# Performance work log

Hardware: AMD Instinct MI355X
Metric: run time of the kernel (lower is better)

The kernel has to match this reference:

```python
import jax, jax.numpy as jnp
import numpy as np

HIDDEN = 128   # hidden_dim == input_dim (embedding feeds LSTMCell directly)
OUT = 200000   # output_dim: item catalog size
T = 64         # num_timesteps
K = 50         # num_recommendations
HIST = 200     # length of user history x


def setup_inputs() -> dict:
    key = jax.random.key(0)
    ks = jax.random.split(key, 6)
    s = 0.02
    return {
        "x": jax.random.randint(ks[0], (HIST,), 1, OUT + 1),  # 1-indexed items
        "embed_table": jax.random.normal(ks[1], (OUT, HIDDEN), jnp.float32) * s,
        "W_ih": jax.random.normal(ks[2], (4 * HIDDEN, HIDDEN), jnp.float32) * s,
        "W_hh": jax.random.normal(ks[3], (4 * HIDDEN, HIDDEN), jnp.float32) * s,
        "b_ih": jnp.zeros((4 * HIDDEN,), jnp.float32),
        "b_hh": jnp.zeros((4 * HIDDEN,), jnp.float32),
        "W_out": jax.random.normal(ks[4], (OUT, HIDDEN), jnp.float32) * s,
        "b_out": jnp.zeros((OUT,), jnp.float32),
    }


def reference(x, embed_table, W_ih, W_hh, b_ih, b_hh, W_out, b_out):
    # Faithful translation of RecModel.forward with prev_a_hat=None, prev_feedback=None.
    def step(carry, i):
        h, c, mask, a_hat, feedback = carry
        # at i==0 the embedding input is forced to zeros (feedback starts at 0 anyway)
        emb = jnp.where(i > 0, embed_table[a_hat] * feedback.astype(jnp.float32), 0.0)
        # LSTMCell: gates order (input, forget, cell, output) as in torch
        gates = W_ih @ emb + b_ih + W_hh @ h + b_hh
        ig, fg, gg, og = jnp.split(gates, 4)
        c_new = jax.nn.sigmoid(fg) * c + jax.nn.sigmoid(ig) * jnp.tanh(gg)
        h_new = jax.nn.sigmoid(og) * jnp.tanh(c_new)
        probs = jax.nn.softmax(W_out @ h_new + b_out)  # Softmax(dim=0) on [OUT]
        masked = probs * mask
        _, top_items = jax.lax.top_k(masked, K)
        hit = jnp.isin(top_items + 1, x)               # x is 1-indexed
        any_hit = jnp.any(hit)
        first_hit = top_items[jnp.argmax(hit)]         # first intersecting item
        a_new = jnp.where(any_hit, first_hit, top_items[0]).astype(jnp.int32)
        fb_new = jnp.where(any_hit, 1, -1).astype(jnp.int32)
        mask_new = mask.at[a_new].set(0.0)
        return (h_new, c_new, mask_new, a_new, fb_new), (a_new, fb_new, masked)

    init = (
        jnp.zeros((HIDDEN,), jnp.float32),
        jnp.zeros((HIDDEN,), jnp.float32),
        jnp.ones((OUT,), jnp.float32),
        jnp.array(0, jnp.int32),
        jnp.array(0, jnp.int32),
    )
    _, (a_hats, feedbacks, masked_probs) = jax.lax.scan(step, init, jnp.arange(T))
    return a_hats, feedbacks, masked_probs
```

## Files before the change

### kernel.cpp

```cpp
#include <hip/hip_runtime.h>
#include <stdint.h>

#define OUTN   200000
#define HID    128
#define NSTEP  64
#define KTOP   50
#define NBINS  1024
#define CAP    4096
#define NBLK   256
#define NTHR   512
#define NWRD   6250

__device__ __forceinline__ float    gldf(const float* p){ return __hip_atomic_load(p, __ATOMIC_RELAXED, __HIP_MEMORY_SCOPE_AGENT); }
__device__ __forceinline__ void     gstf(float* p, float v){ __hip_atomic_store(p, v, __ATOMIC_RELAXED, __HIP_MEMORY_SCOPE_AGENT); }
__device__ __forceinline__ unsigned gldu(const unsigned* p){ return __hip_atomic_load(p, __ATOMIC_RELAXED, __HIP_MEMORY_SCOPE_AGENT); }
__device__ __forceinline__ void     gstu(unsigned* p, unsigned v){ __hip_atomic_store(p, v, __ATOMIC_RELAXED, __HIP_MEMORY_SCOPE_AGENT); }

__device__ __forceinline__ float dot128f(const float* __restrict__ w, const float* __restrict__ h){
  const float4* w4 = (const float4*)w;
  float acc = 0.f;
  #pragma unroll
  for (int k=0;k<32;k++){
    float4 q = w4[k];
    const float* hp = h + k*4;
    acc += q.x*hp[0] + q.y*hp[1] + q.z*hp[2] + q.w*hp[3];
  }
  return acc;
}

__device__ __forceinline__ int binOf(float l, float rlo, float rsc){
  float b = (l - rlo) * rsc;
  b = fminf(fmaxf(b, 0.f), (float)(NBINS-1));
  return (int)b;
}

__device__ __forceinline__ void blockRed5(float& mx, float& mn, float& a, float& b, float& c,
                                          int tid, float* sm ){
  #pragma unroll
  for (int o=32;o;o>>=1){
    mx=fmaxf(mx,__shfl_xor(mx,o)); mn=fminf(mn,__shfl_xor(mn,o));
    a+=__shfl_xor(a,o); b+=__shfl_xor(b,o); c+=__shfl_xor(c,o);
  }
  __syncthreads();
  if ((tid&63)==0){ int w=tid>>6; sm[w*5+0]=mx; sm[w*5+1]=mn; sm[w*5+2]=a; sm[w*5+3]=b; sm[w*5+4]=c; }
  __syncthreads();
  int nw = blockDim.x>>6;
  if (tid==0){
    for (int k=1;k<nw;k++){
      sm[0]=fmaxf(sm[0],sm[k*5+0]); sm[1]=fminf(sm[1],sm[k*5+1]);
      sm[2]+=sm[k*5+2]; sm[3]+=sm[k*5+3]; sm[4]+=sm[k*5+4];
    }
  }
  __syncthreads();
  mx=sm[0]; mn=sm[1]; a=sm[2]; b=sm[3]; c=sm[4];
}

__device__ __forceinline__ void blockRedPair(float& p, int& i, int tid, float* smp, int* smi){
  __syncthreads();
  #pragma unroll
  for (int o=32;o;o>>=1){
    float p2=__shfl_xor(p,o); int i2=__shfl_xor(i,o);
    if (p2>p || (p2==p && i2<i)){ p=p2; i=i2; }
  }
  if ((tid&63)==0){ smp[tid>>6]=p; smi[tid>>6]=i; }
  __syncthreads();
  if (tid==0){
    for (int k=1;k<8;k++){
      if (smp[k]>smp[0] || (smp[k]==smp[0] && smi[k]<smi[0])){ smp[0]=smp[k]; smi[0]=smi[k]; }
    }
  }
  __syncthreads();
  p=smp[0]; i=smi[0];
}

__device__ __forceinline__ int blockRedSum(int v, int tid, int* smi){
  __syncthreads();
  #pragma unroll
  for (int o=32;o;o>>=1) v += __shfl_xor(v,o);
  if ((tid&63)==0) smi[tid>>6]=v;
  __syncthreads();
  if (tid==0){ int s=0; for(int k=0;k<8;k++) s+=smi[k]; smi[0]=s; }
  __syncthreads();
  return smi[0];
}

__device__ __forceinline__ void histSelect(unsigned* histL, unsigned* csum, int tid, int K, int* outp){
  int base = NBINS - 2*(tid+1);
  csum[tid] = histL[base] + histL[base+1];
  __syncthreads();
  for (int off=1; off<NTHR; off<<=1){
    unsigned add = (tid>=off) ? csum[tid-off] : 0u;
    __syncthreads();
    csum[tid] += add;
    __syncthreads();
  }
  unsigned pre = (tid==0)?0u:csum[tid-1];
  if (csum[tid] >= (unsigned)K && pre < (unsigned)K){
    unsigned run = pre; int bs = base;
    for (int b=base+1; b>=base; --b){
      run += histL[b];
      if (run >= (unsigned)K){ bs=b; break; }
    }
    outp[0]=bs; outp[1]=(int)run;
  }
  __syncthreads();
}

__device__ __forceinline__ void gsync(unsigned* bar, unsigned target){
  asm volatile("s_waitcnt vmcnt(0) lgkmcnt(0)" ::: "memory");
  __syncthreads();
  if (threadIdx.x==0){
    __hip_atomic_fetch_add(bar, 1u, __ATOMIC_RELAXED, __HIP_MEMORY_SCOPE_AGENT);
    unsigned v;
    do {
      __builtin_amdgcn_s_sleep(2);
      v = __hip_atomic_load(bar, __ATOMIC_RELAXED, __HIP_MEMORY_SCOPE_AGENT);
    } while (v < target);
  }
  __syncthreads();
  asm volatile("" ::: "memory");
}

extern "C" __global__ void k_init(const int* __restrict__ x,
                                  const float* __restrict__ b_ih, const float* __restrict__ b_hh,
                                  unsigned* mask_bits, unsigned* inx_bits, unsigned* hist_g,
                                  unsigned* gcount, float* rparams, float* h_ws, float* c_ws,
                                  unsigned* bar)
{
  int tid = threadIdx.x;
  for (int i=tid;i<NWRD;i+=1024){ mask_bits[i]=0xFFFFFFFFu; inx_bits[i]=0u; }
  for (int i=tid;i<NBINS;i+=1024) hist_g[i]=0u;
  if (tid==0){ *gcount=0u; rparams[0]=0.f; rparams[1]=0.f; *bar=0u; }
  if (tid<HID){
    float ig=b_ih[tid]       +b_hh[tid];
    float gg=b_ih[tid+2*HID] +b_hh[tid+2*HID];
    float og=b_ih[tid+3*HID] +b_hh[tid+3*HID];
    float si=1.f/(1.f+expf(-ig)), so=1.f/(1.f+expf(-og));
    float cn=si*tanhf(gg);
    c_ws[tid]=cn; h_ws[tid]=so*tanhf(cn);
  }
  __syncthreads();
  if (tid<200){
    int v = x[tid]-1;
    if (v>=0 && v<OUTN) atomicOr(&inx_bits[v>>5], 1u<<(v&31));
  }
}

struct FusedP {
  const float* emb;  const float* Wih;  const float* Whh;
  const float* bih;  const float* bhh;  const float* Wout; const float* bout;
  float* out;
  float* l_ws; float* partials;
  unsigned* mask_bits; unsigned* inx_bits; unsigned* hist_g;
  unsigned* cand; unsigned* gcount; float* rparams;
  float* h_ws; float* c_ws; unsigned* bar;
};

extern "C" __global__ void __launch_bounds__(NTHR) k_fused(FusedP p)
{
  __shared__ float    h_l[HID];
  __shared__ float    emb_l[HID];
  __shared__ float    gates[4*HID];
  __shared__ unsigned hl[NBINS];
  __shared__ unsigned csum[NTHR];
  __shared__ float    smf[48];
  __shared__ float    smp[8];
  __shared__ int      smi[8];
  __shared__ int      s_sel[2];
  __shared__ int      s_nc, s_cnt;

  const int tid=threadIdx.x, bid=blockIdx.x;
  const int start = bid*781 + (bid<64 ? bid : 64);
  const int cnt   = 781 + (bid<64 ? 1 : 0);
  unsigned barT = 0;

  for (int t=0; t<NSTEP; ++t){
    if (tid<HID) h_l[tid]=gldf(&p.h_ws[tid]);
    for (int i=tid;i<NBINS;i+=NTHR) hl[i]=0u;
    float rlo = gldf(&p.rparams[0]), rsc = gldf(&p.rparams[1]);
    __syncthreads();
    float mx=-3e38f, mn=3e38f, se=0.f, sl=0.f, sl2=0.f;
    float lv0=0.f, lv1=0.f; unsigned mv0=0u, mv1=0u;
    {
      int j = tid;
      if (j < cnt){
        int row = start+j;
        float l = dot128f(p.Wout+(size_t)row*HID, h_l) + p.bout[row];
        gstf(&p.l_ws[row], l);
        lv0 = l;
        se += expf(l)-1.f; sl += l; sl2 += l*l;
        if ((gldu(&p.mask_bits[row>>5])>>(row&31))&1u){
          mv0 = 1u;
          mx=fmaxf(mx,l); mn=fminf(mn,l);
          if (rsc>0.f) atomicAdd(&hl[binOf(l,rlo,rsc)],1u);
        }
      }
      j = tid + NTHR;
      if (j < cnt){
        int row = start+j;
        float l = dot128f(p.Wout+(size_t)row*HID, h_l) + p.bout[row];
        gstf(&p.l_ws[row], l);
        lv1 = l;
        se += expf(l)-1.f; sl += l; sl2 += l*l;
        if ((gldu(&p.mask_bits[row>>5])>>(row&31))&1u){
          mv1 = 1u;
          mx=fmaxf(mx,l); mn=fminf(mn,l);
          if (rsc>0.f) atomicAdd(&hl[binOf(l,rlo,rsc)],1u);
        }
      }
    }
    blockRed5(mx,mn,se,sl,sl2,tid,smf);
    if (tid==0){
      float* q=&p.partials[bid*8];
      gstf(q+0,mx); gstf(q+1,mn); gstf(q+2,se); gstf(q+3,sl); gstf(q+4,sl2);
    }
    if (rsc>0.f){
      for (int i=tid;i<NBINS;i+=NTHR){ unsigned v=hl[i]; if (v) atomicAdd(&p.hist_g[i],v); }
    }
    barT += NBLK; gsync(p.bar, barT);

    if (!(rsc>0.f)){
      float bmx=-3e38f,bmn=3e38f,bse=0.f,bsl=0.f,bsl2=0.f;
      if (tid<NBLK){
        const float* q=&p.partials[tid*8];
        bmx=gldf(q+0); bmn=gldf(q+1); bse=gldf(q+2); bsl=gldf(q+3); bsl2=gldf(q+4);
      }
      blockRed5(bmx,bmn,bse,bsl,bsl2,tid,smf);
      float mean=bsl/2.0e5f, var=bsl2/2.0e5f-mean*mean, sg=sqrtf(fmaxf(var,0.f));
      rlo = bmx-24.f*sg; rsc = (sg>0.f)?((float)NBINS/(32.f*sg)):0.f;
      if (rsc>0.f){
        for (int i=tid;i<NBINS;i+=NTHR) hl[i]=0u;
        __syncthreads();
        if (mv0) atomicAdd(&hl[binOf(lv0,rlo,rsc)],1u);
        if (mv1) atomicAdd(&hl[binOf(lv1,rlo,rsc)],1u);
        __syncthreads();
        for (int i=tid;i<NBINS;i+=NTHR){ unsigned v=hl[i]; if (v) atomicAdd(&p.hist_g[i],v); }
      }
      barT += NBLK; gsync(p.bar, barT);
    }

    float gmx=-3e38f,gmn=3e38f,gse=0.f,gsl=0.f,gsl2=0.f;
    if (tid<NBLK){
      const float* q=&p.partials[tid*8];
      gmx=gldf(q+0); gmn=gldf(q+1); gse=gldf(q+2); gsl=gldf(q+3); gsl2=gldf(q+4);
    }
    for (int i=tid;i<NBINS;i+=NTHR) hl[i]=gldu(&p.hist_g[i]);
    if (tid==0){ s_sel[0]=NBINS; s_sel[1]=0x7fffffff; }
    blockRed5(gmx,gmn,gse,gsl,gsl2,tid,smf);
    const float invS = 1.f/(2.0e5f + gse);
    histSelect(hl,csum,tid,KTOP,s_sel);
    const int  bstar  = s_sel[0];
    const int  bcnt   = s_sel[1];
    const bool doComp = (bcnt<=CAP) && (rsc>0.f);
    float* orow = p.out + 2*NSTEP + (size_t)t*OUTN;
    {
      int j = tid;
      if (j < cnt){
        int row = start+j;
        __builtin_nontemporal_store(mv0 ? expf(lv0)*invS : 0.f, &orow[row]);
        if (doComp && mv0 && binOf(lv0,rlo,rsc)>=bstar){
          unsigned pos = atomicAdd(p.gcount,1u);
          if (pos<CAP) gstu(&p.cand[pos],(unsigned)row);
        }
      }
      j = tid + NTHR;
      if (j < cnt){
        int row = start+j;
        __builtin_nontemporal_store(mv1 ? expf(lv1)*invS : 0.f, &orow[row]);
        if (doComp && mv1 && binOf(lv1,rlo,rsc)>=bstar){
          unsigned pos = atomicAdd(p.gcount,1u);
          if (pos<CAP) gstu(&p.cand[pos],(unsigned)row);
        }
      }
    }
    barT += NBLK; gsync(p.bar, barT);

    if (bid==0){
      int nc = doComp ? (int)gldu(p.gcount) : 0;
      bool ok = doComp && nc>=KTOP && nc<=CAP;

      if (!ok){
        if (gmn >= gmx){
          if (tid==0){
            int c=0;
            for (int i=0;i<OUTN && c<KTOP;i++)
              if ((gldu(&p.mask_bits[i>>5])>>(i&31))&1u) gstu(&p.cand[c++],(unsigned)i);
            s_nc=c;
          }
        } else {
          for (int i=tid;i<NBINS;i+=NTHR) hl[i]=0u;
          __syncthreads();
          const float sc2 = (float)NBINS/(gmx-gmn);
          for (int i=tid;i<OUTN;i+=NTHR)
            if ((gldu(&p.mask_bits[i>>5])>>(i&31))&1u)
              atomicAdd(&hl[binOf(gldf(&p.l_ws[i]),gmn,sc2)],1u);
          __syncthreads();
          histSelect(hl,csum,tid,KTOP,s_sel);
          int b2=s_sel[0], c2=s_sel[1];
          if (c2<=CAP){
            if (tid==0) s_cnt=0;
            __syncthreads();
            for (int i=tid;i<OUTN;i+=NTHR){
              if ((gldu(&p.mask_bits[i>>5])>>(i&31))&1u && binOf(gldf(&p.l_ws[i]),gmn,sc2)>=b2){
                int q=atomicAdd(&s_cnt,1);
                if (q<CAP) gstu(&p.cand[q],(unsigned)i);
              }
            }
            __syncthreads();
            if (tid==0) s_nc = (s_cnt<CAP ? s_cnt : CAP);
          } else {
            if (tid==0){
              int c=0;
              for (int i=0;i<OUTN && c<KTOP;i++)
                if (((gldu(&p.mask_bits[i>>5])>>(i&31))&1u) && binOf(gldf(&p.l_ws[i]),gmn,sc2)>=b2)
                  gstu(&p.cand[c++],(unsigned)i);
              s_nc=c;
            }
          }
        }
        __syncthreads();
        nc = s_nc;
      }

      float bp=-3.4e38f; int bi=0x7fffffff;
      float hp=-3.4e38f; int hidx=0x7fffffff;
      for (int j=tid;j<nc;j+=NTHR){
        int idx=(int)gldu(&p.cand[j]);
        float l=gldf(&p.l_ws[idx]);
        if (l>bp || (l==bp && idx<bi)){ bp=l; bi=idx; }
        if (((p.inx_bits[idx>>5]>>(idx&31))&1u) && (l>hp || (l==hp && idx<hidx))){ hp=l; hidx=idx; }
      }
      blockRedPair(bp,bi,tid,smp,smi);
      blockRedPair(hp,hidx,tid,smp,smi);
      int a, fb;
      if (hidx != 0x7fffffff){
        int better=0;
        for (int j=tid;j<nc;j+=NTHR){
          int idx=(int)gldu(&p.cand[j]);
          float l=gldf(&p.l_ws[idx]);
          better += (l>hp || (l==hp && idx<hidx)) ? 1 : 0;
        }
        better = blockRedSum(better,tid,smi);
        if (better < KTOP){ a=hidx; fb=1; } else { a=bi; fb=-1; }
      } else { a=bi; fb=-1; }
      if (a<0 || a>=OUTN) a=0;

      if (tid==0){
        p.out[t]       = (float)a;
        p.out[NSTEP+t] = (float)fb;
        atomicAnd(&p.mask_bits[a>>5], ~(1u<<(a&31)));
      }

      if (tid<HID) emb_l[tid]=p.emb[(size_t)a*HID+tid] * (float)fb;
      __syncthreads();
      float g = dot128f(p.Wih+(size_t)tid*HID, emb_l) + dot128f(p.Whh+(size_t)tid*HID, h_l)
              + p.bih[tid] + p.bhh[tid];
      gates[tid]=g;
      __syncthreads();
      if (tid<HID){
        float ig=gates[tid], fg=gates[tid+HID], gg=gates[tid+2*HID], og=gates[tid+3*HID];
        float si=1.f/(1.f+expf(-ig)), sf=1.f/(1.f+expf(-fg)), so=1.f/(1.f+expf(-og));
        float cn=sf*gldf(&p.c_ws[tid])+si*tanhf(gg);
        float hn=so*tanhf(cn);
        gstf(&p.c_ws[tid],cn); gstf(&p.h_ws[tid],hn);
      }

      if (tid==0){
        gstu(p.gcount,0u);
        float mean=gsl/2.0e5f;
        float var =gsl2/2.0e5f - mean*mean;
        float sg  =sqrtf(fmaxf(var,0.f));
        gstf(&p.rparams[0],gmx-24.f*sg);
        gstf(&p.rparams[1],(sg>0.f)?((float)NBINS/(32.f*sg)):0.f);
      }
    } else if (bid==1){
      for (int i=tid;i<NBINS;i+=NTHR) gstu(&p.hist_g[i],0u);
    }
    barT += NBLK; gsync(p.bar, barT);
  }
}

extern "C" void kernel_launch(void* const* d_in, const int* in_sizes, int n_in,
                              void* d_out, int out_size, void* d_ws, size_t ws_size,
                              hipStream_t stream)
{
  const int*   x    = (const int*)d_in[0];
  const float* emb  = (const float*)d_in[1];
  const float* Wih  = (const float*)d_in[2];
  const float* Whh  = (const float*)d_in[3];
  const float* bih  = (const float*)d_in[4];
  const float* bhh  = (const float*)d_in[5];
  const float* Wout = (const float*)d_in[6];
  const float* bout = (const float*)d_in[7];
  float* out = (float*)d_out;

  char* ws = (char*)d_ws;
  float*    l_ws      = (float*)(ws + 0);
  float*    partials  = (float*)(ws + 800000);
  unsigned* mask_bits = (unsigned*)(ws + 808192);
  unsigned* inx_bits  = (unsigned*)(ws + 833280);
  unsigned* hist_g    = (unsigned*)(ws + 858368);
  unsigned* cand      = (unsigned*)(ws + 862464);
  unsigned* gcount    = (unsigned*)(ws + 878848);
  unsigned* bar       = (unsigned*)(ws + 878976);
  float*    rparams   = (float*)(ws + 879104);
  float*    h_ws      = (float*)(ws + 879360);
  float*    c_ws      = (float*)(ws + 879872);

  hipLaunchKernelGGL(k_init, dim3(1), dim3(1024), 0, stream,
                     x, bih, bhh, mask_bits, inx_bits, hist_g, gcount, rparams, h_ws, c_ws, bar);

  FusedP p;
  p.emb=emb; p.Wih=Wih; p.Whh=Whh; p.bih=bih; p.bhh=bhh; p.Wout=Wout; p.bout=bout;
  p.out=out; p.l_ws=l_ws; p.partials=partials;
  p.mask_bits=mask_bits; p.inx_bits=inx_bits; p.hist_g=hist_g;
  p.cand=cand; p.gcount=gcount; p.rparams=rparams;
  p.h_ws=h_ws; p.c_ws=c_ws; p.bar=bar;

  void* args[] = { &p };
  hipLaunchCooperativeKernel((const void*)k_fused, dim3(NBLK), dim3(NTHR), args, 0, stream);
}
```

Measured before the change: 4.265 ms.

## Use per-block local top-K candidates and hierarchical grid barrier to cut syncs

Each block now builds its own histogram over its local logit range and emits up to 64 packed (logit,index) candidates, so block 0 can pick the top-1 and first hit without a global histogram pass. This removes one or two of the grid barriers per step. The masked-probability row is written one step late, using a published inverse sum, so the extra barrier for normalisation disappears. The flat atomic barrier is replaced by a two-level group arrive/release barrier to reduce contention. In exchange the kernel carries more register state, adds a fallback path for when a block overflows its 64 candidate slots, and has more complex cross-step dependencies.

Measured after the change: 5.133 ms. +20.4%, slower.

```diff
diff --git a/kernel.cpp b/kernel.cpp
--- a/kernel.cpp
+++ b/kernel.cpp
@@ -10,11 +10,16 @@
 #define NBLK   256
 #define NTHR   512
 #define NWRD   6250
+#define GRP    8
+#define GSZ    32
+#define SLOTS  64
 
 __device__ __forceinline__ float    gldf(const float* p){ return __hip_atomic_load(p, __ATOMIC_RELAXED, __HIP_MEMORY_SCOPE_AGENT); }
 __device__ __forceinline__ void     gstf(float* p, float v){ __hip_atomic_store(p, v, __ATOMIC_RELAXED, __HIP_MEMORY_SCOPE_AGENT); }
 __device__ __forceinline__ unsigned gldu(const unsigned* p){ return __hip_atomic_load(p, __ATOMIC_RELAXED, __HIP_MEMORY_SCOPE_AGENT); }
 __device__ __forceinline__ void     gstu(unsigned* p, unsigned v){ __hip_atomic_store(p, v, __ATOMIC_RELAXED, __HIP_MEMORY_SCOPE_AGENT); }
+__device__ __forceinline__ unsigned long long gld64(const unsigned long long* p){ return __hip_atomic_load(p, __ATOMIC_RELAXED, __HIP_MEMORY_SCOPE_AGENT); }
+__device__ __forceinline__ void     gst64(unsigned long long* p, unsigned long long v){ __hip_atomic_store(p, v, __ATOMIC_RELAXED, __HIP_MEMORY_SCOPE_AGENT); }
 
 __device__ __forceinline__ float dot128f(const float* __restrict__ w, const float* __restrict__ h){
   const float4* w4 = (const float4*)w;
@@ -34,25 +39,22 @@
   return (int)b;
 }
 
-__device__ __forceinline__ void blockRed5(float& mx, float& mn, float& a, float& b, float& c,
-                                          int tid, float* sm ){
+__device__ __forceinline__ void blockRed3(float& mx, float& mn, float& a, int tid, float* sm ){
+  __syncthreads();
   #pragma unroll
   for (int o=32;o;o>>=1){
     mx=fmaxf(mx,__shfl_xor(mx,o)); mn=fminf(mn,__shfl_xor(mn,o));
-    a+=__shfl_xor(a,o); b+=__shfl_xor(b,o); c+=__shfl_xor(c,o);
-  }
-  __syncthreads();
-  if ((tid&63)==0){ int w=tid>>6; sm[w*5+0]=mx; sm[w*5+1]=mn; sm[w*5+2]=a; sm[w*5+3]=b; sm[w*5+4]=c; }
-  __syncthreads();
-  int nw = blockDim.x>>6;
+    a+=__shfl_xor(a,o);
+  }
+  if ((tid&63)==0){ int w=tid>>6; sm[w*3+0]=mx; sm[w*3+1]=mn; sm[w*3+2]=a; }
+  __syncthreads();
   if (tid==0){
-    for (int k=1;k<nw;k++){
-      sm[0]=fmaxf(sm[0],sm[k*5+0]); sm[1]=fminf(sm[1],sm[k*5+1]);
-      sm[2]+=sm[k*5+2]; sm[3]+=sm[k*5+3]; sm[4]+=sm[k*5+4];
-    }
-  }
-  __syncthreads();
-  mx=sm[0]; mn=sm[1]; a=sm[2]; b=sm[3]; c=sm[4];
+    for (int k=1;k<8;k++){
+      sm[0]=fmaxf(sm[0],sm[k*3+0]); sm[1]=fminf(sm[1],sm[k*3+1]); sm[2]+=sm[k*3+2];
+    }
+  }
+  __syncthreads();
+  mx=sm[0]; mn=sm[1]; a=sm[2];
 }
 
 __device__ __forceinline__ void blockRedPair(float& p, int& i, int tid, float* smp, int* smi){
@@ -103,19 +105,27 @@
     }
     outp[0]=bs; outp[1]=(int)run;
   }
-  __syncthreads();
-}
-
-__device__ __forceinline__ void gsync(unsigned* bar, unsigned target){
+  if (tid==NTHR-1 && csum[tid] < (unsigned)K){ outp[0]=0; outp[1]=(int)csum[tid]; }
+  __syncthreads();
+}
+
+__device__ __forceinline__ void gsync(unsigned* garr, unsigned* gctr, unsigned* grel,
+                                      int bid, unsigned s){
   asm volatile("s_waitcnt vmcnt(0) lgkmcnt(0)" ::: "memory");
   __syncthreads();
   if (threadIdx.x==0){
-    __hip_atomic_fetch_add(bar, 1u, __ATOMIC_RELAXED, __HIP_MEMORY_SCOPE_AGENT);
-    unsigned v;
-    do {
+    int g = bid>>5;
+    unsigned r = __hip_atomic_fetch_add(garr+g*64, 1u, __ATOMIC_RELAXED, __HIP_MEMORY_SCOPE_AGENT);
+    if (r == s*GSZ-1u){
+      unsigned q = __hip_atomic_fetch_add(gctr, 1u, __ATOMIC_RELAXED, __HIP_MEMORY_SCOPE_AGENT);
+      if (q == s*GRP-1u){
+        #pragma unroll
+        for (int k=0;k<GRP;k++)
+          __hip_atomic_store(grel+k*64, s, __ATOMIC_RELAXED, __HIP_MEMORY_SCOPE_AGENT);
+      }
+    }
+    while (__hip_atomic_load(grel+g*64, __ATOMIC_RELAXED, __HIP_MEMORY_SCOPE_AGENT) < s)
       __builtin_amdgcn_s_sleep(2);
-      v = __hip_atomic_load(bar, __ATOMIC_RELAXED, __HIP_MEMORY_SCOPE_AGENT);
-    } while (v < target);
   }
   __syncthreads();
   asm volatile("" ::: "memory");
@@ -123,14 +133,15 @@
 
 extern "C" __global__ void k_init(const int* __restrict__ x,
                                   const float* __restrict__ b_ih, const float* __restrict__ b_hh,
-                                  unsigned* mask_bits, unsigned* inx_bits, unsigned* hist_g,
-                                  unsigned* gcount, float* rparams, float* h_ws, float* c_ws,
-                                  unsigned* bar)
+                                  unsigned* mask_bits, unsigned* inx_bits,
+                                  float* pubInv, float* h_ws, float* c_ws,
+                                  unsigned* garr, unsigned* gctr, unsigned* grel)
 {
   int tid = threadIdx.x;
   for (int i=tid;i<NWRD;i+=1024){ mask_bits[i]=0xFFFFFFFFu; inx_bits[i]=0u; }
-  for (int i=tid;i<NBINS;i+=1024) hist_g[i]=0u;
-  if (tid==0){ *gcount=0u; rparams[0]=0.f; rparams[1]=0.f; *bar=0u; }
+  for (int i=tid;i<GRP*64;i+=1024){ garr[i]=0u; grel[i]=0u; }
+  if (tid<64) gctr[tid]=0u;
+  if (tid==0) pubInv[0]=0.f;
   if (tid<HID){
     float ig=b_ih[tid]       +b_hh[tid];
     float gg=b_ih[tid+2*HID] +b_hh[tid+2*HID];
@@ -151,9 +162,10 @@
   const float* bih;  const float* bhh;  const float* Wout; const float* bout;
   float* out;
   float* l_ws; float* partials;
-  unsigned* mask_bits; unsigned* inx_bits; unsigned* hist_g;
-  unsigned* cand; unsigned* gcount; float* rparams;
-  float* h_ws; float* c_ws; unsigned* bar;
+  unsigned* mask_bits; unsigned* inx_bits;
+  unsigned* cntb; unsigned long long* cand;
+  float* pubInv; float* h_ws; float* c_ws;
+  unsigned* garr; unsigned* gctr; unsigned* grel;
 };
 
 extern "C" __global__ void __launch_bounds__(NTHR) k_fused(FusedP p)
@@ -161,136 +173,169 @@
   __shared__ float    h_l[HID];
   __shared__ float    emb_l[HID];
   __shared__ float    gates[4*HID];
+  __shared__ float    c_l[HID];
+  __shared__ unsigned m_l[32];
   __shared__ unsigned hl[NBINS];
   __shared__ unsigned csum[NTHR];
-  __shared__ float    smf[48];
+  __shared__ unsigned cnt_l[NBLK];
+  __shared__ float    smf[24];
   __shared__ float    smp[8];
   __shared__ int      smi[8];
   __shared__ int      s_sel[2];
-  __shared__ int      s_nc, s_cnt;
+  __shared__ int      s_nc, s_cnt, s_flag;
 
   const int tid=threadIdx.x, bid=blockIdx.x;
   const int start = bid*781 + (bid<64 ? bid : 64);
   const int cnt   = 781 + (bid<64 ? 1 : 0);
-  unsigned barT = 0;
+  const int w_lo  = start>>5;
+  const int nw    = ((start+cnt-1)>>5) - w_lo + 1;
+  unsigned bs = 0;
+
+  if (bid==0 && tid<HID) c_l[tid]=gldf(&p.c_ws[tid]);
+
+  float lv0=0.f, lv1=0.f; unsigned mv0=0u, mv1=0u;
 
   for (int t=0; t<NSTEP; ++t){
     if (tid<HID) h_l[tid]=gldf(&p.h_ws[tid]);
+    if (tid<nw)  m_l[tid]=gldu(&p.mask_bits[w_lo+tid]);
     for (int i=tid;i<NBINS;i+=NTHR) hl[i]=0u;
-    float rlo = gldf(&p.rparams[0]), rsc = gldf(&p.rparams[1]);
+    const float invSp = gldf(p.pubInv);
     __syncthreads();
-    float mx=-3e38f, mn=3e38f, se=0.f, sl=0.f, sl2=0.f;
-    float lv0=0.f, lv1=0.f; unsigned mv0=0u, mv1=0u;
+
+    float mx=-3e38f, mn=3e38f, se=0.f;
+    float* orowp = p.out + 2*NSTEP + (size_t)(t-1)*OUTN;
     {
-      int j = tid;
-      if (j < cnt){
-        int row = start+j;
+      int j=tid;
+      if (j<cnt){
+        int row=start+j;
+        if (t>0) __builtin_nontemporal_store(mv0 ? expf(lv0)*invSp : 0.f, &orowp[row]);
         float l = dot128f(p.Wout+(size_t)row*HID, h_l) + p.bout[row];
         gstf(&p.l_ws[row], l);
-        lv0 = l;
-        se += expf(l)-1.f; sl += l; sl2 += l*l;
-        if ((gldu(&p.mask_bits[row>>5])>>(row&31))&1u){
-          mv0 = 1u;
-          mx=fmaxf(mx,l); mn=fminf(mn,l);
-          if (rsc>0.f) atomicAdd(&hl[binOf(l,rlo,rsc)],1u);
-        }
-      }
-      j = tid + NTHR;
-      if (j < cnt){
-        int row = start+j;
+        lv0=l; se += expf(l)-1.f;
+        mv0 = (m_l[(row>>5)-w_lo]>>(row&31))&1u;
+        if (mv0){ mx=fmaxf(mx,l); mn=fminf(mn,l); }
+      } else { mv0=0u; }
+      j=tid+NTHR;
+      if (j<cnt){
+        int row=start+j;
+        if (t>0) __builtin_nontemporal_store(mv1 ? expf(lv1)*invSp : 0.f, &orowp[row]);
         float l = dot128f(p.Wout+(size_t)row*HID, h_l) + p.bout[row];
         gstf(&p.l_ws[row], l);
-        lv1 = l;
-        se += expf(l)-1.f; sl += l; sl2 += l*l;
-        if ((gldu(&p.mask_bits[row>>5])>>(row&31))&1u){
-          mv1 = 1u;
-          mx=fmaxf(mx,l); mn=fminf(mn,l);
-          if (rsc>0.f) atomicAdd(&hl[binOf(l,rlo,rsc)],1u);
-        }
-      }
-    }
-    blockRed5(mx,mn,se,sl,sl2,tid,smf);
-    if (tid==0){
-      float* q=&p.partials[bid*8];
-      gstf(q+0,mx); gstf(q+1,mn); gstf(q+2,se); gstf(q+3,sl); gstf(q+4,sl2);
-    }
-    if (rsc>0.f){
-      for (int i=tid;i<NBINS;i+=NTHR){ unsigned v=hl[i]; if (v) atomicAdd(&p.hist_g[i],v); }
-    }
-    barT += NBLK; gsync(p.bar, barT);
-
-    if (!(rsc>0.f)){
-      float bmx=-3e38f,bmn=3e38f,bse=0.f,bsl=0.f,bsl2=0.f;
+        lv1=l; se += expf(l)-1.f;
+        mv1 = (m_l[(row>>5)-w_lo]>>(row&31))&1u;
+        if (mv1){ mx=fmaxf(mx,l); mn=fminf(mn,l); }
+      } else { mv1=0u; }
+    }
+    blockRed3(mx,mn,se,tid,smf);
+    if (tid==0){ float* q=&p.partials[bid*4]; gstf(q,mx); gstf(q+1,mn); gstf(q+2,se); }
+
+    const bool okloc = (mx>mn);
+    if (okloc){
+      const float rsc=(float)NBINS/(mx-mn);
+      if (mv0) atomicAdd(&hl[binOf(lv0,mn,rsc)],1u);
+      if (mv1) atomicAdd(&hl[binOf(lv1,mn,rsc)],1u);
+      if (tid==0){ s_cnt=0; s_sel[0]=NBINS; s_sel[1]=0; }
+      __syncthreads();
+      histSelect(hl,csum,tid,KTOP,s_sel);
+      const int bstar=s_sel[0];
+      if (mv0 && binOf(lv0,mn,rsc)>=bstar){
+        int pos=atomicAdd(&s_cnt,1);
+        if (pos<SLOTS){
+          int row=start+tid;
+          gst64(&p.cand[bid*SLOTS+pos],
+                ((unsigned long long)__float_as_uint(lv0)<<32)|(unsigned)row);
+        }
+      }
+      if (mv1 && binOf(lv1,mn,rsc)>=bstar){
+        int pos=atomicAdd(&s_cnt,1);
+        if (pos<SLOTS){
+          int row=start+tid+NTHR;
+          gst64(&p.cand[bid*SLOTS+pos],
+                ((unsigned long long)__float_as_uint(lv1)<<32)|(unsigned)row);
+        }
+      }
+      __syncthreads();
+      if (tid==0) gstu(&p.cntb[bid],(unsigned)s_cnt);
+    } else {
+      if (tid==0) gstu(&p.cntb[bid],0x7fffffffu);
+    }
+    ++bs; gsync(p.garr,p.gctr,p.grel,bid,bs);
+
+    if (bid==0){
+      float gmx=-3e38f,gmn=3e38f,gse=0.f;
       if (tid<NBLK){
-        const float* q=&p.partials[tid*8];
-        bmx=gldf(q+0); bmn=gldf(q+1); bse=gldf(q+2); bsl=gldf(q+3); bsl2=gldf(q+4);
-      }
-      blockRed5(bmx,bmn,bse,bsl,bsl2,tid,smf);
-      float mean=bsl/2.0e5f, var=bsl2/2.0e5f-mean*mean, sg=sqrtf(fmaxf(var,0.f));
-      rlo = bmx-24.f*sg; rsc = (sg>0.f)?((float)NBINS/(32.f*sg)):0.f;
-      if (rsc>0.f){
-        for (int i=tid;i<NBINS;i+=NTHR) hl[i]=0u;
-        __syncthreads();
-        if (mv0) atomicAdd(&hl[binOf(lv0,rlo,rsc)],1u);
-        if (mv1) atomicAdd(&hl[binOf(lv1,rlo,rsc)],1u);
-        __syncthreads();
-        for (int i=tid;i<NBINS;i+=NTHR){ unsigned v=hl[i]; if (v) atomicAdd(&p.hist_g[i],v); }
-      }
-      barT += NBLK; gsync(p.bar, barT);
-    }
-
-    float gmx=-3e38f,gmn=3e38f,gse=0.f,gsl=0.f,gsl2=0.f;
-    if (tid<NBLK){
-      const float* q=&p.partials[tid*8];
-      gmx=gldf(q+0); gmn=gldf(q+1); gse=gldf(q+2); gsl=gldf(q+3); gsl2=gldf(q+4);
-    }
-    for (int i=tid;i<NBINS;i+=NTHR) hl[i]=gldu(&p.hist_g[i]);
-    if (tid==0){ s_sel[0]=NBINS; s_sel[1]=0x7fffffff; }
-    blockRed5(gmx,gmn,gse,gsl,gsl2,tid,smf);
-    const float invS = 1.f/(2.0e5f + gse);
-    histSelect(hl,csum,tid,KTOP,s_sel);
-    const int  bstar  = s_sel[0];
-    const int  bcnt   = s_sel[1];
-    const bool doComp = (bcnt<=CAP) && (rsc>0.f);
-    float* orow = p.out + 2*NSTEP + (size_t)t*OUTN;
-    {
-      int j = tid;
-      if (j < cnt){
-        int row = start+j;
-        __builtin_nontemporal_store(mv0 ? expf(lv0)*invS : 0.f, &orow[row]);
-        if (doComp && mv0 && binOf(lv0,rlo,rsc)>=bstar){
-          unsigned pos = atomicAdd(p.gcount,1u);
-          if (pos<CAP) gstu(&p.cand[pos],(unsigned)row);
-        }
-      }
-      j = tid + NTHR;
-      if (j < cnt){
-        int row = start+j;
-        __builtin_nontemporal_store(mv1 ? expf(lv1)*invS : 0.f, &orow[row]);
-        if (doComp && mv1 && binOf(lv1,rlo,rsc)>=bstar){
-          unsigned pos = atomicAdd(p.gcount,1u);
-          if (pos<CAP) gstu(&p.cand[pos],(unsigned)row);
-        }
-      }
-    }
-    barT += NBLK; gsync(p.bar, barT);
-
-    if (bid==0){
-      int nc = doComp ? (int)gldu(p.gcount) : 0;
-      bool ok = doComp && nc>=KTOP && nc<=CAP;
-
-      if (!ok){
-        if (gmn >= gmx){
-          if (tid==0){
-            int c=0;
-            for (int i=0;i<OUTN && c<KTOP;i++)
-              if ((gldu(&p.mask_bits[i>>5])>>(i&31))&1u) gstu(&p.cand[c++],(unsigned)i);
-            s_nc=c;
-          }
+        const float* q=&p.partials[tid*4];
+        gmx=gldf(q); gmn=gldf(q+1); gse=gldf(q+2);
+        cnt_l[tid]=gldu(&p.cntb[tid]);
+      }
+      blockRed3(gmx,gmn,gse,tid,smf);
+      const float invS = 1.f/(2.0e5f+gse);
+      if (tid==0) s_flag=0;
+      __syncthreads();
+      if (tid<NBLK && cnt_l[tid]>SLOTS) s_flag=1;
+      __syncthreads();
+      int a, fb;
+      if (!s_flag){
+        unsigned long long sv[32]; unsigned um=0u;
+        #pragma unroll
+        for (int k=0;k<32;k++){
+          int j=tid+k*NTHR; int b=j>>6, s=j&63;
+          if (s < (int)cnt_l[b]){ sv[k]=gld64(&p.cand[j]); um|=1u<<k; }
+          else sv[k]=0ull;
+        }
+        float bp=-3.4e38f; int bi=0x7fffffff;
+        float hp=-3.4e38f; int hidx=0x7fffffff;
+        #pragma unroll
+        for (int k=0;k<32;k++){
+          if ((um>>k)&1u){
+            int idx=(int)(unsigned)(sv[k]&0xffffffffu);
+            float l=__uint_as_float((unsigned)(sv[k]>>32));
+            if (l>bp || (l==bp && idx<bi)){ bp=l; bi=idx; }
+            if (((p.inx_bits[idx>>5]>>(idx&31))&1u) && (l>hp || (l==hp && idx<hidx))){ hp=l; hidx=idx; }
+          }
+        }
+        blockRedPair(bp,bi,tid,smp,smi);
+        blockRedPair(hp,hidx,tid,smp,smi);
+        if (hidx != 0x7fffffff){
+          int better=0;
+          #pragma unroll
+          for (int k=0;k<32;k++){
+            if ((um>>k)&1u){
+              int idx=(int)(unsigned)(sv[k]&0xffffffffu);
+              float l=__uint_as_float((unsigned)(sv[k]>>32));
+              better += (l>hp || (l==hp && idx<hidx)) ? 1 : 0;
+            }
+          }
+          better=blockRedSum(better,tid,smi);
+          if (better<KTOP){ a=hidx; fb=1; } else { a=bi; fb=-1; }
+        } else { a=bi; fb=-1; }
+      } else {
+        unsigned* candf=(unsigned*)p.cand;
+        int nc;
+        if (gmn>=gmx){
+          unsigned w=gldu(&p.mask_bits[tid]);
+          hl[tid]=w; csum[tid]=(unsigned)__popc(w);
+          __syncthreads();
+          for (int off=1; off<NTHR; off<<=1){
+            unsigned add=(tid>=off)?csum[tid-off]:0u;
+            __syncthreads();
+            csum[tid]+=add;
+            __syncthreads();
+          }
+          unsigned pre = tid? csum[tid-1]:0u;
+          if (pre<(unsigned)KTOP){
+            unsigned word=hl[tid]; unsigned r=pre;
+            for (int b2=0;b2<32 && r<(unsigned)KTOP;b2++){
+              if ((word>>b2)&1u){ gstu(&candf[r],(unsigned)(tid*32+b2)); r++; }
+            }
+          }
+          __syncthreads();
+          nc = (int)(csum[NTHR-1]<(unsigned)KTOP ? csum[NTHR-1] : (unsigned)KTOP);
         } else {
           for (int i=tid;i<NBINS;i+=NTHR) hl[i]=0u;
+          if (tid==0){ s_sel[0]=NBINS; s_sel[1]=0; }
           __syncthreads();
-          const float sc2 = (float)NBINS/(gmx-gmn);
+          const float sc2=(float)NBINS/(gmx-gmn);
           for (int i=tid;i<OUTN;i+=NTHR)
             if ((gldu(&p.mask_bits[i>>5])>>(i&31))&1u)
               atomicAdd(&hl[binOf(gldf(&p.l_ws[i]),gmn,sc2)],1u);
@@ -303,55 +348,53 @@
             for (int i=tid;i<OUTN;i+=NTHR){
               if ((gldu(&p.mask_bits[i>>5])>>(i&31))&1u && binOf(gldf(&p.l_ws[i]),gmn,sc2)>=b2){
                 int q=atomicAdd(&s_cnt,1);
-                if (q<CAP) gstu(&p.cand[q],(unsigned)i);
+                if (q<CAP) gstu(&candf[q],(unsigned)i);
               }
             }
             __syncthreads();
-            if (tid==0) s_nc = (s_cnt<CAP ? s_cnt : CAP);
+            nc = (s_cnt<CAP ? s_cnt : CAP);
           } else {
             if (tid==0){
               int c=0;
               for (int i=0;i<OUTN && c<KTOP;i++)
                 if (((gldu(&p.mask_bits[i>>5])>>(i&31))&1u) && binOf(gldf(&p.l_ws[i]),gmn,sc2)>=b2)
-                  gstu(&p.cand[c++],(unsigned)i);
+                  gstu(&candf[c++],(unsigned)i);
               s_nc=c;
             }
-          }
-        }
-        __syncthreads();
-        nc = s_nc;
-      }
-
-      float bp=-3.4e38f; int bi=0x7fffffff;
-      float hp=-3.4e38f; int hidx=0x7fffffff;
-      for (int j=tid;j<nc;j+=NTHR){
-        int idx=(int)gldu(&p.cand[j]);
-        float l=gldf(&p.l_ws[idx]);
-        if (l>bp || (l==bp && idx<bi)){ bp=l; bi=idx; }
-        if (((p.inx_bits[idx>>5]>>(idx&31))&1u) && (l>hp || (l==hp && idx<hidx))){ hp=l; hidx=idx; }
-      }
-      blockRedPair(bp,bi,tid,smp,smi);
-      blockRedPair(hp,hidx,tid,smp,smi);
-      int a, fb;
-      if (hidx != 0x7fffffff){
-        int better=0;
+            __syncthreads();
+            nc=s_nc;
+          }
+        }
+        float bp=-3.4e38f; int bi=0x7fffffff;
+        float hp=-3.4e38f; int hidx=0x7fffffff;
         for (int j=tid;j<nc;j+=NTHR){
-          int idx=(int)gldu(&p.cand[j]);
+          int idx=(int)gldu(&candf[j]);
           float l=gldf(&p.l_ws[idx]);
-          better += (l>hp || (l==hp && idx<hidx)) ? 1 : 0;
-        }
-        better = blockRedSum(better,tid,smi);
-        if (better < KTOP){ a=hidx; fb=1; } else { a=bi; fb=-1; }
-      } else { a=bi; fb=-1; }
+          if (l>bp || (l==bp && idx<bi)){ bp=l; bi=idx; }
+          if (((p.inx_bits[idx>>5]>>(idx&31))&1u) && (l>hp || (l==hp && idx<hidx))){ hp=l; hidx=idx; }
+        }
+        blockRedPair(bp,bi,tid,smp,smi);
+        blockRedPair(hp,hidx,tid,smp,smi);
+        if (hidx != 0x7fffffff){
+          int better=0;
+          for (int j=tid;j<nc;j+=NTHR){
+            int idx=(int)gldu(&candf[j]);
+            float l=gldf(&p.l_ws[idx]);
+            better += (l>hp || (l==hp && idx<hidx)) ? 1 : 0;
+          }
+          better=blockRedSum(better,tid,smi);
+          if (better<KTOP){ a=hidx; fb=1; } else { a=bi; fb=-1; }
+        } else { a=bi; fb=-1; }
+      }
       if (a<0 || a>=OUTN) a=0;
 
       if (tid==0){
         p.out[t]       = (float)a;
         p.out[NSTEP+t] = (float)fb;
         atomicAnd(&p.mask_bits[a>>5], ~(1u<<(a&31)));
-      }
-
-      if (tid<HID) emb_l[tid]=p.emb[(size_t)a*HID+tid] * (float)fb;
+        gstf(p.pubInv, invS);
+      }
+      if (tid<HID) emb_l[tid]=p.emb[(size_t)a*HID+tid]*(float)fb;
       __syncthreads();
       float g = dot128f(p.Wih+(size_t)tid*HID, emb_l) + dot128f(p.Whh+(size_t)tid*HID, h_l)
               + p.bih[tid] + p.bhh[tid];
@@ -360,23 +403,21 @@
       if (tid<HID){
         float ig=gates[tid], fg=gates[tid+HID], gg=gates[tid+2*HID], og=gates[tid+3*HID];
         float si=1.f/(1.f+expf(-ig)), sf=1.f/(1.f+expf(-fg)), so=1.f/(1.f+expf(-og));
-        float cn=sf*gldf(&p.c_ws[tid])+si*tanhf(gg);
+        float cn=sf*c_l[tid]+si*tanhf(gg);
         float hn=so*tanhf(cn);
-        gstf(&p.c_ws[tid],cn); gstf(&p.h_ws[tid],hn);
-      }
-
-      if (tid==0){
-        gstu(p.gcount,0u);
-        float mean=gsl/2.0e5f;
-        float var =gsl2/2.0e5f - mean*mean;
-        float sg  =sqrtf(fmaxf(var,0.f));
-        gstf(&p.rparams[0],gmx-24.f*sg);
-        gstf(&p.rparams[1],(sg>0.f)?((float)NBINS/(32.f*sg)):0.f);
-      }
-    } else if (bid==1){
-      for (int i=tid;i<NBINS;i+=NTHR) gstu(&p.hist_g[i],0u);
-    }
-    barT += NBLK; gsync(p.bar, barT);
+        c_l[tid]=cn; gstf(&p.h_ws[tid],hn);
+      }
+    }
+    ++bs; gsync(p.garr,p.gctr,p.grel,bid,bs);
+  }
+
+  {
+    const float invSL = gldf(p.pubInv);
+    float* orow = p.out + 2*NSTEP + (size_t)(NSTEP-1)*OUTN;
+    int j=tid;
+    if (j<cnt){ int row=start+j; __builtin_nontemporal_store(mv0 ? expf(lv0)*invSL : 0.f, &orow[row]); }
+    j=tid+NTHR;
+    if (j<cnt){ int row=start+j; __builtin_nontemporal_store(mv1 ? expf(lv1)*invSL : 0.f, &orow[row]); }
   }
 }
 
@@ -396,26 +437,28 @@
 
   char* ws = (char*)d_ws;
   float*    l_ws      = (float*)(ws + 0);
-  float*    partials  = (float*)(ws + 800000);
-  unsigned* mask_bits = (unsigned*)(ws + 808192);
-  unsigned* inx_bits  = (unsigned*)(ws + 833280);
-  unsigned* hist_g    = (unsigned*)(ws + 858368);
-  unsigned* cand      = (unsigned*)(ws + 862464);
-  unsigned* gcount    = (unsigned*)(ws + 878848);
-  unsigned* bar       = (unsigned*)(ws + 878976);
-  float*    rparams   = (float*)(ws + 879104);
-  float*    h_ws      = (float*)(ws + 879360);
-  float*    c_ws      = (float*)(ws + 879872);
+  float*    partials  = (float*)(ws + 800256);
+  unsigned* mask_bits = (unsigned*)(ws + 804352);
+  unsigned* inx_bits  = (unsigned*)(ws + 829440);
+  unsigned* cntb      = (unsigned*)(ws + 854528);
+  unsigned long long* cand = (unsigned long long*)(ws + 855552);
+  unsigned* garr      = (unsigned*)(ws + 986624);
+  unsigned* gctr      = (unsigned*)(ws + 988672);
+  unsigned* grel      = (unsigned*)(ws + 988928);
+  float*    pubInv    = (float*)(ws + 990976);
+  float*    h_ws      = (float*)(ws + 991232);
+  float*    c_ws      = (float*)(ws + 991744);
 
   hipLaunchKernelGGL(k_init, dim3(1), dim3(1024), 0, stream,
-                     x, bih, bhh, mask_bits, inx_bits, hist_g, gcount, rparams, h_ws, c_ws, bar);
+                     x, bih, bhh, mask_bits, inx_bits, pubInv, h_ws, c_ws, garr, gctr, grel);
 
   FusedP p;
   p.emb=emb; p.Wih=Wih; p.Whh=Whh; p.bih=bih; p.bhh=bhh; p.Wout=Wout; p.bout=bout;
   p.out=out; p.l_ws=l_ws; p.partials=partials;
-  p.mask_bits=mask_bits; p.inx_bits=inx_bits; p.hist_g=hist_g;
-  p.cand=cand; p.gcount=gcount; p.rparams=rparams;
-  p.h_ws=h_ws; p.c_ws=c_ws; p.bar=bar;
+  p.mask_bits=mask_bits; p.inx_bits=inx_bits;
+  p.cntb=cntb; p.cand=cand;
+  p.pubInv=pubInv; p.h_ws=h_ws; p.c_ws=c_ws;
+  p.garr=garr; p.gctr=gctr; p.grel=grel;
 
   void* args[] = { &p };
   hipLaunchCooperativeKernel((const void*)k_fused, dim3(NBLK), dim3(NTHR), args, 0, stream);
```
